# Kernel optimization log

Measured on AMD Instinct MI355X. Metric: run time of the kernel, lower is better.

The kernel has to match this reference:

```python
import jax, jax.numpy as jnp
import numpy as np

HIDDEN = 2048
HEADS = 16
HEAD_DIM = HIDDEN // HEADS
ROPE_BASE = 10000.0
BSZ, SEQ = 1, 2048
F32_MIN = jnp.finfo(jnp.float32).min


def setup_inputs() -> dict:
    key = jax.random.key(0)
    ks = jax.random.split(key, 5)
    hidden_states = jax.random.normal(ks[0], (BSZ, SEQ, HIDDEN), dtype=jnp.float32)
    # causal additive mask: 0 on/below diagonal, large negative above
    causal = jnp.tril(jnp.ones((SEQ, SEQ), dtype=bool))
    attention_mask = jnp.where(causal, 0.0, F32_MIN)[None, None, :, :].astype(jnp.float32)
    position_ids = jnp.broadcast_to(jnp.arange(SEQ, dtype=jnp.int32)[None, :], (BSZ, SEQ))
    scale = 1.0 / np.sqrt(HIDDEN)
    Wq = jax.random.normal(ks[1], (HIDDEN, HIDDEN), dtype=jnp.float32) * scale
    Wk = jax.random.normal(ks[2], (HIDDEN, HIDDEN), dtype=jnp.float32) * scale
    Wv = jax.random.normal(ks[3], (HIDDEN, HIDDEN), dtype=jnp.float32) * scale
    Wo = jax.random.normal(ks[4], (HIDDEN, HIDDEN), dtype=jnp.float32) * scale
    return {"hidden_states": hidden_states, "attention_mask": attention_mask,
            "position_ids": position_ids, "Wq": Wq, "Wk": Wk, "Wv": Wv, "Wo": Wo}


def _rotate_half(x):
    x1, x2 = jnp.split(x, 2, axis=-1)
    return jnp.concatenate([-x2, x1], axis=-1)


def _rope_cos_sin(position_ids, dtype):
    # [b, s] int -> cos/sin [b, 1, s, head_dim]
    inv_freq = 1.0 / (ROPE_BASE ** (jnp.arange(0, HEAD_DIM, 2, dtype=jnp.float32) / HEAD_DIM))
    freqs = position_ids.astype(jnp.float32)[..., None] * inv_freq  # [b, s, d/2]
    emb = jnp.concatenate([freqs, freqs], axis=-1)  # [b, s, d]
    return jnp.cos(emb)[:, None].astype(dtype), jnp.sin(emb)[:, None].astype(dtype)


def reference(hidden_states, attention_mask, position_ids, Wq, Wk, Wv, Wo):
    b, s, _ = hidden_states.shape

    def proj(W):  # [b, s, hidden] -> [b, h, s, d]
        return jnp.einsum('bsm,mn->bsn', hidden_states, W).reshape(b, s, HEADS, HEAD_DIM).transpose(0, 2, 1, 3)

    q, k, v = proj(Wq), proj(Wk), proj(Wv)
    cos, sin = _rope_cos_sin(position_ids, q.dtype)
    q = q * cos + _rotate_half(q) * sin
    k = k * cos + _rotate_half(k) * sin

    scores = jnp.einsum('bhqd,bhkd->bhqk', q, k) / np.sqrt(HEAD_DIM)
    scores = jnp.maximum(scores + attention_mask, F32_MIN)
    attn = jax.nn.softmax(scores.astype(jnp.float32), axis=-1).astype(q.dtype)
    out = jnp.einsum('bhqk,bhkd->bhqd', attn, v)  # [b, h, s, d]
    out = out.transpose(0, 2, 1, 3).reshape(b, s, HIDDEN)
    return jnp.einsum('bsm,mn->bsn', out, Wo)
```

## Files before the change

### kernel.cpp

```cpp
#include <hip/hip_runtime.h>
#include <hip/hip_bf16.h>
#include <math.h>

#define SEQn 2048
#define HID  2048
#define NH   16
#define HD   128

typedef __attribute__((ext_vector_type(8))) __bf16 bf16x8;
typedef __attribute__((ext_vector_type(4))) float  f32x4;

#define MFMA16(a,b,c) __builtin_amdgcn_mfma_f32_16x16x32_bf16((a),(b),(c),0,0,0)

__device__ __forceinline__ ushort f2bf(float f) {
  union { float f; unsigned u; } v; v.f = f;
  unsigned r = v.u + 0x7fffu + ((v.u >> 16) & 1u);
  return (ushort)(r >> 16);
}
__device__ __forceinline__ float bf2f(ushort u) {
  union { unsigned u; float f; } v; v.u = ((unsigned)u) << 16; return v.f;
}
__device__ __forceinline__ void split2(float x, ushort& h, ushort& l) {
  h = f2bf(x);
  l = f2bf(x - bf2f(h));
}
__device__ __forceinline__ void gl_lds16(const ushort* g, ushort* l) {
  __builtin_amdgcn_global_load_lds((const __attribute__((address_space(1))) unsigned int*)g,
                                   (__attribute__((address_space(3))) unsigned int*)l, 16, 0, 0);
}

__global__ void k_rope_tables(const int* __restrict__ pos,
                              float* __restrict__ cosT, float* __restrict__ sinT) {
  int t = threadIdx.x;
  int s = blockIdx.x * 4 + (t >> 6), i = t & 63;
  float p = (float)pos[s];
  float ex = (float)(2 * i) / 128.0f;
  float invf = 1.0f / powf(10000.0f, ex);
  float f = p * invf;
  cosT[s * 64 + i] = cosf(f);
  sinT[s * 64 + i] = sinf(f);
}

__global__ void k_split(const float* __restrict__ x,
                        ushort* __restrict__ hi, ushort* __restrict__ lo, int n4) {
  int i = blockIdx.x * blockDim.x + threadIdx.x;
  if (i >= n4) return;
  const float4 v = ((const float4*)x)[i];
  ushort4 h, l;
  split2(v.x, h.x, l.x); split2(v.y, h.y, l.y);
  split2(v.z, h.z, l.z); split2(v.w, h.w, l.w);
  ((ushort4*)hi)[i] = h; ((ushort4*)lo)[i] = l;
}

__global__ void k_splitT3(const float* __restrict__ W0, const float* __restrict__ W1,
                          const float* __restrict__ W2,
                          ushort* __restrict__ Th, ushort* __restrict__ Tl) {
  __shared__ float tile[32][33];
  const float* W = (blockIdx.z == 0) ? W0 : (blockIdx.z == 1) ? W1 : W2;
  ushort* Thz = Th + (size_t)blockIdx.z * HID * HID;
  ushort* Tlz = Tl + (size_t)blockIdx.z * HID * HID;
  int kb = blockIdx.x * 32, nb = blockIdx.y * 32;
  int tx = threadIdx.x, ty = threadIdx.y;
#pragma unroll
  for (int r = 0; r < 4; r++)
    tile[ty + r * 8][tx] = W[(size_t)(kb + ty + r * 8) * HID + nb + tx];
  __syncthreads();
#pragma unroll
  for (int r = 0; r < 4; r++) {
    int n = nb + ty + r * 8, k = kb + tx;
    ushort h, l; split2(tile[tx][ty + r * 8], h, l);
    Thz[(size_t)n * HID + k] = h;
    Tlz[(size_t)n * HID + k] = l;
  }
}

__global__ __launch_bounds__(512) void k_gemm_x3(
    const ushort* __restrict__ Ah, const ushort* __restrict__ Al,
    const ushort* __restrict__ Bh, const ushort* __restrict__ Bl,
    float* __restrict__ C) {
  __shared__ alignas(16) ushort lds[4][128 * 32];
  const int t = threadIdx.x, lane = t & 63, w = t >> 6;
  const int bm = blockIdx.y * 128, bn = blockIdx.x * 128;
  const size_t zb = (size_t)blockIdx.z * HID * HID;
  const int lr = lane & 15, lg = lane >> 4;
  const int sr = t >> 2, sc = (t & 3) * 8;
  const ushort* ga  = Ah + (size_t)(bm + sr) * HID + sc;
  const ushort* gal = Al + (size_t)(bm + sr) * HID + sc;
  const ushort* gb  = Bh + zb + (size_t)(bn + sr) * HID + sc;
  const ushort* gbl = Bl + zb + (size_t)(bn + sr) * HID + sc;
  ushort* l0 = &lds[0][w * 512];
  ushort* l1 = &lds[1][w * 512];
  ushort* l2 = &lds[2][w * 512];
  ushort* l3 = &lds[3][w * 512];
  const int wr = (w & 3) * 32, wc = (w >> 2) * 64;
  f32x4 acc[2][4] = {};
  for (int k0 = 0; k0 < HID; k0 += 32) {
    __syncthreads();
    gl_lds16(ga  + k0, l0);
    gl_lds16(gal + k0, l1);
    gl_lds16(gb  + k0, l2);
    gl_lds16(gbl + k0, l3);
    __syncthreads();
    bf16x8 a_h[2], a_l[2], b_h[4], b_l[4];
#pragma unroll
    for (int mi = 0; mi < 2; mi++) {
      int ro = (wr + mi * 16 + lr) * 32 + lg * 8;
      a_h[mi] = *(const bf16x8*)&lds[0][ro];
      a_l[mi] = *(const bf16x8*)&lds[1][ro];
    }
#pragma unroll
    for (int ni = 0; ni < 4; ni++) {
      int ro = (wc + ni * 16 + lr) * 32 + lg * 8;
      b_h[ni] = *(const bf16x8*)&lds[2][ro];
      b_l[ni] = *(const bf16x8*)&lds[3][ro];
    }
#pragma unroll
    for (int mi = 0; mi < 2; mi++)
#pragma unroll
      for (int ni = 0; ni < 4; ni++) {
        acc[mi][ni] = MFMA16(a_h[mi], b_h[ni], acc[mi][ni]);
        acc[mi][ni] = MFMA16(a_h[mi], b_l[ni], acc[mi][ni]);
        acc[mi][ni] = MFMA16(a_l[mi], b_h[ni], acc[mi][ni]);
      }
  }
  float* Cz = C + (size_t)blockIdx.z * SEQn * HID;
#pragma unroll
  for (int mi = 0; mi < 2; mi++)
#pragma unroll
    for (int ni = 0; ni < 4; ni++)
#pragma unroll
      for (int j = 0; j < 4; j++) {
        int row = bm + wr + mi * 16 + lg * 4 + j;
        int col = bn + wc + ni * 16 + lr;
        Cz[(size_t)row * HID + col] = acc[mi][ni][j];
      }
}

__global__ void k_rope_qk(const float* __restrict__ Qf, const float* __restrict__ Kf,
                          const float* __restrict__ cosT, const float* __restrict__ sinT,
                          ushort* __restrict__ Qhh, ushort* __restrict__ Qll,
                          ushort* __restrict__ Khh, ushort* __restrict__ Kll) {
  int t = threadIdx.x;
  int s = blockIdx.x * 4 + (t >> 6), h = blockIdx.y, d = t & 63;
  const float scale = 0.08838834764831845f;
  float c = cosT[s * 64 + d], sn = sinT[s * 64 + d];
  size_t in0  = (size_t)s * HID + h * HD + d;
  size_t out0 = ((size_t)h * SEQn + s) * HD + d;
  ushort hh, ll;
  {
    float q1 = Qf[in0] * scale, q2 = Qf[in0 + 64] * scale;
    split2(q1 * c - q2 * sn, hh, ll); Qhh[out0] = hh;      Qll[out0] = ll;
    split2(q2 * c + q1 * sn, hh, ll); Qhh[out0 + 64] = hh; Qll[out0 + 64] = ll;
  }
  {
    float k1 = Kf[in0], k2 = Kf[in0 + 64];
    split2(k1 * c - k2 * sn, hh, ll); Khh[out0] = hh;      Kll[out0] = ll;
    split2(k2 * c + k1 * sn, hh, ll); Khh[out0 + 64] = hh; Kll[out0 + 64] = ll;
  }
}

__global__ void k_transpose_v(const float* __restrict__ Vf,
                              ushort* __restrict__ Vth, ushort* __restrict__ Vtl) {
  __shared__ float tile[32][33];
  int h = blockIdx.x, db = blockIdx.y * 32, sb = blockIdx.z * 32;
  int tx = threadIdx.x, ty = threadIdx.y;
#pragma unroll
  for (int r = 0; r < 4; r++)
    tile[ty + r * 8][tx] = Vf[(size_t)(sb + ty + r * 8) * HID + h * HD + db + tx];
  __syncthreads();
#pragma unroll
  for (int r = 0; r < 4; r++) {
    int d = db + ty + r * 8, s = sb + tx;
    ushort hh, ll; split2(tile[tx][ty + r * 8], hh, ll);
    size_t o = ((size_t)h * HD + d) * SEQn + s;
    Vth[o] = hh; Vtl[o] = ll;
  }
}

__global__ __launch_bounds__(256) void k_attn(
    const ushort* __restrict__ Qhh, const ushort* __restrict__ Qll,
    const ushort* __restrict__ Khh, const ushort* __restrict__ Kll,
    const ushort* __restrict__ Vth, const ushort* __restrict__ Vtl,
    ushort* __restrict__ Ohi, ushort* __restrict__ Olo) {
  __shared__ alignas(16) ushort sKh[64 * 128];
  __shared__ alignas(16) ushort sKl[64 * 128];
  __shared__ alignas(16) ushort sVh[128 * 64];
  __shared__ alignas(16) ushort sVl[128 * 64];
  __shared__ alignas(16) ushort sP[4][16 * 72];
  const int t = threadIdx.x, lane = t & 63, w = t >> 6;
  const int flat = blockIdx.y * 32 + blockIdx.x;
  const int s_ = flat & 255, halfsel = flat >> 8;
  const int qt_ = s_ & 31, h_ = s_ >> 5;
  const int qt = halfsel ? (31 - qt_) : qt_;
  const int h  = halfsel ? (8 + h_) : h_;
  const int qb = qt * 64;
  const int lr = lane & 15, lg = lane >> 4;
  const int q0 = qb + w * 16;
  const size_t qoff = ((size_t)h * SEQn + q0 + lr) * HD + lg * 8;
  bf16x8 qh[4], ql[4];
#pragma unroll
  for (int ks = 0; ks < 4; ks++) {
    qh[ks] = *(const bf16x8*)(Qhh + qoff + ks * 32);
    ql[ks] = *(const bf16x8*)(Qll + qoff + ks * 32);
  }
  const int cc = (w << 6) | lane;
  const int rK = cc >> 4;
  const int cbK = (((cc & 15) << 4) ^ ((rK & 7) << 4)) >> 1;
  const size_t srcKo = (size_t)(h * SEQn + rK) * HD + cbK;
  const int rV = cc >> 3;
  const int cbV = (((cc & 7) << 4) ^ ((rV & 7) << 4)) >> 1;
  const size_t srcVo = (size_t)(h * HD + rV) * SEQn + cbV;

  f32x4 o[8] = {};
  float mrow[4], lrow[4];
#pragma unroll
  for (int j = 0; j < 4; j++) { mrow[j] = -INFINITY; lrow[j] = 0.f; }
  ushort* myp = &sP[w][0];

  for (int kv0 = 0; kv0 <= qb; kv0 += 64) {
    __syncthreads();
    {
      const ushort* gKh = Khh + srcKo + (size_t)kv0 * HD;
      const ushort* gKl = Kll + srcKo + (size_t)kv0 * HD;
      const ushort* gVh = Vth + srcVo + kv0;
      const ushort* gVl = Vtl + srcVo + kv0;
#pragma unroll
      for (int i = 0; i < 4; i++) {
        gl_lds16(gKh + (size_t)i * 16 * HD,  &sKh[(w + i * 4) * 512]);
        gl_lds16(gKl + (size_t)i * 16 * HD,  &sKl[(w + i * 4) * 512]);
        gl_lds16(gVh + (size_t)i * 32 * SEQn, &sVh[(w + i * 4) * 512]);
        gl_lds16(gVl + (size_t)i * 32 * SEQn, &sVl[(w + i * 4) * 512]);
      }
    }
    __syncthreads();
    f32x4 s4[4] = {};
    __builtin_amdgcn_s_setprio(1);
#pragma unroll
    for (int ni = 0; ni < 4; ni++) {
      const int kr = ni * 16 + lr;
      const int kbase = kr * 128;
      const int ksw = (kr & 7) << 4;
#pragma unroll
      for (int ks = 0; ks < 4; ks++) {
        const int off = kbase + (((ks * 64 + lg * 16) ^ ksw) >> 1);
        bf16x8 kh = *(const bf16x8*)&sKh[off];
        bf16x8 kl = *(const bf16x8*)&sKl[off];
        s4[ni] = MFMA16(qh[ks], kh, s4[ni]);
        s4[ni] = MFMA16(qh[ks], kl, s4[ni]);
        s4[ni] = MFMA16(ql[ks], kh, s4[ni]);
      }
    }
    __builtin_amdgcn_s_setprio(0);
    float sf[4];
    ushort pl[4][4];
#pragma unroll
    for (int j = 0; j < 4; j++) {
      const int row = q0 + lg * 4 + j;
      float sc[4];
#pragma unroll
      for (int ni = 0; ni < 4; ni++) {
        int col = kv0 + ni * 16 + lr;
        sc[ni] = (col <= row) ? s4[ni][j] : -INFINITY;
      }
      float rm = fmaxf(fmaxf(sc[0], sc[1]), fmaxf(sc[2], sc[3]));
#pragma unroll
      for (int off = 1; off < 16; off <<= 1) rm = fmaxf(rm, __shfl_xor(rm, off));
      float mn = fmaxf(mrow[j], rm);
      sf[j] = __expf(mrow[j] - mn);
      float rs = 0.f;
#pragma unroll
      for (int ni = 0; ni < 4; ni++) {
        float pv = __expf(sc[ni] - mn);
        rs += pv;
        ushort hh, ll; split2(pv, hh, ll);
        myp[(lg * 4 + j) * 72 + ni * 16 + lr] = hh;
        pl[j][ni] = ll;
      }
#pragma unroll
      for (int off = 1; off < 16; off <<= 1) rs += __shfl_xor(rs, off);
      lrow[j] = lrow[j] * sf[j] + rs;
      mrow[j] = mn;
    }
#pragma unroll
    for (int nn = 0; nn < 8; nn++) {
      o[nn][0] *= sf[0]; o[nn][1] *= sf[1]; o[nn][2] *= sf[2]; o[nn][3] *= sf[3];
    }
    bf16x8 p0h = *(const bf16x8*)&myp[lr * 72 + lg * 8];
    bf16x8 p1h = *(const bf16x8*)&myp[lr * 72 + lg * 8 + 32];
#pragma unroll
    for (int j = 0; j < 4; j++)
#pragma unroll
      for (int ni = 0; ni < 4; ni++)
        myp[(lg * 4 + j) * 72 + ni * 16 + lr] = pl[j][ni];
    bf16x8 p0l = *(const bf16x8*)&myp[lr * 72 + lg * 8];
    bf16x8 p1l = *(const bf16x8*)&myp[lr * 72 + lg * 8 + 32];
    __builtin_amdgcn_s_setprio(1);
#pragma unroll
    for (int nn = 0; nn < 8; nn++) {
      const int d = nn * 16 + lr;
      const int vbase = d * 64;
      const int vsw = (d & 7) << 4;
      const int o0 = vbase + (((lg * 16) ^ vsw) >> 1);
      const int o1 = vbase + (((lg * 16 + 64) ^ vsw) >> 1);
      bf16x8 vh0 = *(const bf16x8*)&sVh[o0];
      bf16x8 vl0 = *(const bf16x8*)&sVl[o0];
      bf16x8 vh1 = *(const bf16x8*)&sVh[o1];
      bf16x8 vl1 = *(const bf16x8*)&sVl[o1];
      o[nn] = MFMA16(p0h, vh0, o[nn]);
      o[nn] = MFMA16(p0h, vl0, o[nn]);
      o[nn] = MFMA16(p0l, vh0, o[nn]);
      o[nn] = MFMA16(p1h, vh1, o[nn]);
      o[nn] = MFMA16(p1h, vl1, o[nn]);
      o[nn] = MFMA16(p1l, vh1, o[nn]);
    }
    __builtin_amdgcn_s_setprio(0);
  }
#pragma unroll
  for (int nn = 0; nn < 8; nn++)
#pragma unroll
    for (int j = 0; j < 4; j++) {
      int row = q0 + lg * 4 + j;
      int col = h * HD + nn * 16 + lr;
      ushort hh, ll; split2(o[nn][j] / lrow[j], hh, ll);
      Ohi[(size_t)row * HID + col] = hh;
      Olo[(size_t)row * HID + col] = ll;
    }
}

extern "C" void kernel_launch(void* const* d_in, const int* in_sizes, int n_in,
                              void* d_out, int out_size, void* d_ws, size_t ws_size,
                              hipStream_t stream) {
  const float* Hf  = (const float*)d_in[0];
  const int*   pos = (const int*)d_in[2];
  const float* Wq  = (const float*)d_in[3];
  const float* Wk  = (const float*)d_in[4];
  const float* Wv  = (const float*)d_in[5];
  const float* Wo  = (const float*)d_in[6];

  char* ws = (char*)d_ws;
  const size_t SZ_TBL = (size_t)SEQn * 64 * 4;
  const size_t SZ_BF  = (size_t)SEQn * HID * 2;
  const size_t SZ_F   = (size_t)SEQn * HID * 4;
  const size_t PLANE  = (size_t)HID * HID;
  size_t off = 0;
  float*  cosT = (float*)(ws + off);  off += SZ_TBL;
  float*  sinT = (float*)(ws + off);  off += SZ_TBL;
  ushort* Hhi  = (ushort*)(ws + off); off += SZ_BF;
  ushort* Hlo  = (ushort*)(ws + off); off += SZ_BF;
  ushort* W3h  = (ushort*)(ws + off); off += 3 * SZ_BF;
  ushort* W3l  = (ushort*)(ws + off); off += 3 * SZ_BF;
  float*  QKVf = (float*)(ws + off);  off += 3 * SZ_F;
  float*  Qf = QKVf;
  float*  Kf = QKVf + (size_t)SEQn * HID;
  float*  Vf = QKVf + 2 * (size_t)SEQn * HID;
  ushort* Qhh = W3h;
  ushort* Qll = W3h + PLANE;
  ushort* Khh = W3h + 2 * PLANE;
  ushort* Kll = W3l;
  ushort* Vth = W3l + PLANE;
  ushort* Vtl = W3l + 2 * PLANE;
  ushort* Ohi = (ushort*)Kf;
  ushort* Olo = (ushort*)((char*)Kf + SZ_BF);

  const int n4 = SEQn * HID / 4;

  k_rope_tables<<<dim3(SEQn / 4), dim3(256), 0, stream>>>(pos, cosT, sinT);
  k_split<<<dim3(n4 / 256), dim3(256), 0, stream>>>(Hf, Hhi, Hlo, n4);

  k_splitT3<<<dim3(64, 64, 3), dim3(32, 8), 0, stream>>>(Wq, Wk, Wv, W3h, W3l);

  k_gemm_x3<<<dim3(16, 16, 3), dim3(512), 0, stream>>>(Hhi, Hlo, W3h, W3l, QKVf);

  k_rope_qk<<<dim3(SEQn / 4, NH), dim3(256), 0, stream>>>(Qf, Kf, cosT, sinT, Qhh, Qll, Khh, Kll);
  k_transpose_v<<<dim3(NH, 4, 64), dim3(32, 8), 0, stream>>>(Vf, Vth, Vtl);

  k_attn<<<dim3(SEQn / 64, NH), dim3(256), 0, stream>>>(Qhh, Qll, Khh, Kll, Vth, Vtl, Ohi, Olo);

  k_splitT3<<<dim3(64, 64, 1), dim3(32, 8), 0, stream>>>(Wo, Wo, Wo, W3h, W3l);
  k_gemm_x3<<<dim3(16, 16, 1), dim3(512), 0, stream>>>(Ohi, Olo, W3h, W3l, (float*)d_out);
}
```

Baseline: 518.1 us.

## Double-buffer LDS tiles in attention and output-projection GEMM to overlap loads

Adds ping-pong LDS buffers to the attention kernel for K and V tiles, and to a templated GEMM variant used only for the output projection. Each iteration now prefetches the next tile while computing on the current one, leaving a single barrier per iteration instead of two. The aim is to hide global-to-LDS load latency behind MFMA work. The attention kernel's LDS roughly doubles, to about 137KB per block, which may cut resident blocks per CU and reduce latency hiding from occupancy. The QKV GEMM keeps the original single-buffer path.

```diff
diff --git a/kernel.cpp b/kernel.cpp
--- a/kernel.cpp
+++ b/kernel.cpp
@@ -74,11 +74,12 @@
   }
 }
 
+template<int DB>
 __global__ __launch_bounds__(512) void k_gemm_x3(
     const ushort* __restrict__ Ah, const ushort* __restrict__ Al,
     const ushort* __restrict__ Bh, const ushort* __restrict__ Bl,
     float* __restrict__ C) {
-  __shared__ alignas(16) ushort lds[4][128 * 32];
+  __shared__ alignas(16) ushort lds[DB][4][4096];
   const int t = threadIdx.x, lane = t & 63, w = t >> 6;
   const int bm = blockIdx.y * 128, bn = blockIdx.x * 128;
   const size_t zb = (size_t)blockIdx.z * HID * HID;
@@ -88,31 +89,43 @@
   const ushort* gal = Al + (size_t)(bm + sr) * HID + sc;
   const ushort* gb  = Bh + zb + (size_t)(bn + sr) * HID + sc;
   const ushort* gbl = Bl + zb + (size_t)(bn + sr) * HID + sc;
-  ushort* l0 = &lds[0][w * 512];
-  ushort* l1 = &lds[1][w * 512];
-  ushort* l2 = &lds[2][w * 512];
-  ushort* l3 = &lds[3][w * 512];
   const int wr = (w & 3) * 32, wc = (w >> 2) * 64;
   f32x4 acc[2][4] = {};
+  int cur = 0;
+  if constexpr (DB == 2) {
+    gl_lds16(ga,  &lds[0][0][w * 512]);
+    gl_lds16(gal, &lds[0][1][w * 512]);
+    gl_lds16(gb,  &lds[0][2][w * 512]);
+    gl_lds16(gbl, &lds[0][3][w * 512]);
+  }
   for (int k0 = 0; k0 < HID; k0 += 32) {
     __syncthreads();
-    gl_lds16(ga  + k0, l0);
-    gl_lds16(gal + k0, l1);
-    gl_lds16(gb  + k0, l2);
-    gl_lds16(gbl + k0, l3);
-    __syncthreads();
+    if constexpr (DB == 2) {
+      if (k0 + 32 < HID) {
+        gl_lds16(ga  + k0 + 32, &lds[cur ^ 1][0][w * 512]);
+        gl_lds16(gal + k0 + 32, &lds[cur ^ 1][1][w * 512]);
+        gl_lds16(gb  + k0 + 32, &lds[cur ^ 1][2][w * 512]);
+        gl_lds16(gbl + k0 + 32, &lds[cur ^ 1][3][w * 512]);
+      }
+    } else {
+      gl_lds16(ga  + k0, &lds[0][0][w * 512]);
+      gl_lds16(gal + k0, &lds[0][1][w * 512]);
+      gl_lds16(gb  + k0, &lds[0][2][w * 512]);
+      gl_lds16(gbl + k0, &lds[0][3][w * 512]);
+      __syncthreads();
+    }
     bf16x8 a_h[2], a_l[2], b_h[4], b_l[4];
 #pragma unroll
     for (int mi = 0; mi < 2; mi++) {
       int ro = (wr + mi * 16 + lr) * 32 + lg * 8;
-      a_h[mi] = *(const bf16x8*)&lds[0][ro];
-      a_l[mi] = *(const bf16x8*)&lds[1][ro];
+      a_h[mi] = *(const bf16x8*)&lds[cur][0][ro];
+      a_l[mi] = *(const bf16x8*)&lds[cur][1][ro];
     }
 #pragma unroll
     for (int ni = 0; ni < 4; ni++) {
       int ro = (wc + ni * 16 + lr) * 32 + lg * 8;
-      b_h[ni] = *(const bf16x8*)&lds[2][ro];
-      b_l[ni] = *(const bf16x8*)&lds[3][ro];
+      b_h[ni] = *(const bf16x8*)&lds[cur][2][ro];
+      b_l[ni] = *(const bf16x8*)&lds[cur][3][ro];
     }
 #pragma unroll
     for (int mi = 0; mi < 2; mi++)
@@ -122,6 +135,7 @@
         acc[mi][ni] = MFMA16(a_h[mi], b_l[ni], acc[mi][ni]);
         acc[mi][ni] = MFMA16(a_l[mi], b_h[ni], acc[mi][ni]);
       }
+    if constexpr (DB == 2) cur ^= 1;
   }
   float* Cz = C + (size_t)blockIdx.z * SEQn * HID;
 #pragma unroll
@@ -182,11 +196,11 @@
     const ushort* __restrict__ Khh, const ushort* __restrict__ Kll,
     const ushort* __restrict__ Vth, const ushort* __restrict__ Vtl,
     ushort* __restrict__ Ohi, ushort* __restrict__ Olo) {
-  __shared__ alignas(16) ushort sKh[64 * 128];
-  __shared__ alignas(16) ushort sKl[64 * 128];
-  __shared__ alignas(16) ushort sVh[128 * 64];
-  __shared__ alignas(16) ushort sVl[128 * 64];
-  __shared__ alignas(16) ushort sP[4][16 * 72];
+  __shared__ alignas(16) ushort sKh[2][8192];
+  __shared__ alignas(16) ushort sKl[2][8192];
+  __shared__ alignas(16) ushort sVh[2][8192];
+  __shared__ alignas(16) ushort sVl[2][8192];
+  __shared__ alignas(16) ushort sP[4][1152];
   const int t = threadIdx.x, lane = t & 63, w = t >> 6;
   const int flat = blockIdx.y * 32 + blockIdx.x;
   const int s_ = flat & 255, halfsel = flat >> 8;
@@ -217,22 +231,36 @@
   for (int j = 0; j < 4; j++) { mrow[j] = -INFINITY; lrow[j] = 0.f; }
   ushort* myp = &sP[w][0];
 
+  {
+    const ushort* gKh = Khh + srcKo;
+    const ushort* gKl = Kll + srcKo;
+    const ushort* gVh = Vth + srcVo;
+    const ushort* gVl = Vtl + srcVo;
+#pragma unroll
+    for (int i = 0; i < 4; i++) {
+      gl_lds16(gKh + (size_t)i * 16 * HD,   &sKh[0][(w + i * 4) * 512]);
+      gl_lds16(gKl + (size_t)i * 16 * HD,   &sKl[0][(w + i * 4) * 512]);
+      gl_lds16(gVh + (size_t)i * 32 * SEQn, &sVh[0][(w + i * 4) * 512]);
+      gl_lds16(gVl + (size_t)i * 32 * SEQn, &sVl[0][(w + i * 4) * 512]);
+    }
+  }
+
   for (int kv0 = 0; kv0 <= qb; kv0 += 64) {
+    const int cur = (kv0 >> 6) & 1;
     __syncthreads();
-    {
-      const ushort* gKh = Khh + srcKo + (size_t)kv0 * HD;
-      const ushort* gKl = Kll + srcKo + (size_t)kv0 * HD;
-      const ushort* gVh = Vth + srcVo + kv0;
-      const ushort* gVl = Vtl + srcVo + kv0;
+    if (kv0 + 64 <= qb) {
+      const ushort* gKh = Khh + srcKo + (size_t)(kv0 + 64) * HD;
+      const ushort* gKl = Kll + srcKo + (size_t)(kv0 + 64) * HD;
+      const ushort* gVh = Vth + srcVo + kv0 + 64;
+      const ushort* gVl = Vtl + srcVo + kv0 + 64;
 #pragma unroll
       for (int i = 0; i < 4; i++) {
-        gl_lds16(gKh + (size_t)i * 16 * HD,  &sKh[(w + i * 4) * 512]);
-        gl_lds16(gKl + (size_t)i * 16 * HD,  &sKl[(w + i * 4) * 512]);
-        gl_lds16(gVh + (size_t)i * 32 * SEQn, &sVh[(w + i * 4) * 512]);
-        gl_lds16(gVl + (size_t)i * 32 * SEQn, &sVl[(w + i * 4) * 512]);
-      }
-    }
-    __syncthreads();
+        gl_lds16(gKh + (size_t)i * 16 * HD,   &sKh[cur ^ 1][(w + i * 4) * 512]);
+        gl_lds16(gKl + (size_t)i * 16 * HD,   &sKl[cur ^ 1][(w + i * 4) * 512]);
+        gl_lds16(gVh + (size_t)i * 32 * SEQn, &sVh[cur ^ 1][(w + i * 4) * 512]);
+        gl_lds16(gVl + (size_t)i * 32 * SEQn, &sVl[cur ^ 1][(w + i * 4) * 512]);
+      }
+    }
     f32x4 s4[4] = {};
     __builtin_amdgcn_s_setprio(1);
 #pragma unroll
@@ -243,8 +271,8 @@
 #pragma unroll
       for (int ks = 0; ks < 4; ks++) {
         const int off = kbase + (((ks * 64 + lg * 16) ^ ksw) >> 1);
-        bf16x8 kh = *(const bf16x8*)&sKh[off];
-        bf16x8 kl = *(const bf16x8*)&sKl[off];
+        bf16x8 kh = *(const bf16x8*)&sKh[cur][off];
+        bf16x8 kl = *(const bf16x8*)&sKl[cur][off];
         s4[ni] = MFMA16(qh[ks], kh, s4[ni]);
         s4[ni] = MFMA16(qh[ks], kl, s4[ni]);
         s4[ni] = MFMA16(ql[ks], kh, s4[ni]);
@@ -302,10 +330,10 @@
       const int vsw = (d & 7) << 4;
       const int o0 = vbase + (((lg * 16) ^ vsw) >> 1);
       const int o1 = vbase + (((lg * 16 + 64) ^ vsw) >> 1);
-      bf16x8 vh0 = *(const bf16x8*)&sVh[o0];
-      bf16x8 vl0 = *(const bf16x8*)&sVl[o0];
-      bf16x8 vh1 = *(const bf16x8*)&sVh[o1];
-      bf16x8 vl1 = *(const bf16x8*)&sVl[o1];
+      bf16x8 vh0 = *(const bf16x8*)&sVh[cur][o0];
+      bf16x8 vl0 = *(const bf16x8*)&sVl[cur][o0];
+      bf16x8 vh1 = *(const bf16x8*)&sVh[cur][o1];
+      bf16x8 vl1 = *(const bf16x8*)&sVl[cur][o1];
       o[nn] = MFMA16(p0h, vh0, o[nn]);
       o[nn] = MFMA16(p0h, vl0, o[nn]);
       o[nn] = MFMA16(p0l, vh0, o[nn]);
@@ -369,7 +397,7 @@
 
   k_splitT3<<<dim3(64, 64, 3), dim3(32, 8), 0, stream>>>(Wq, Wk, Wv, W3h, W3l);
 
-  k_gemm_x3<<<dim3(16, 16, 3), dim3(512), 0, stream>>>(Hhi, Hlo, W3h, W3l, QKVf);
+  k_gemm_x3<1><<<dim3(16, 16, 3), dim3(512), 0, stream>>>(Hhi, Hlo, W3h, W3l, QKVf);
 
   k_rope_qk<<<dim3(SEQn / 4, NH), dim3(256), 0, stream>>>(Qf, Kf, cosT, sinT, Qhh, Qll, Khh, Kll);
   k_transpose_v<<<dim3(NH, 4, 64), dim3(32, 8), 0, stream>>>(Vf, Vth, Vtl);
@@ -377,5 +405,5 @@
   k_attn<<<dim3(SEQn / 64, NH), dim3(256), 0, stream>>>(Qhh, Qll, Khh, Kll, Vth, Vtl, Ohi, Olo);
 
   k_splitT3<<<dim3(64, 64, 1), dim3(32, 8), 0, stream>>>(Wo, Wo, Wo, W3h, W3l);
-  k_gemm_x3<<<dim3(16, 16, 1), dim3(512), 0, stream>>>(Ohi, Olo, W3h, W3l, (float*)d_out);
-}
+  k_gemm_x3<2><<<dim3(16, 16, 1), dim3(512), 0, stream>>>(Ohi, Olo, W3h, W3l, (float*)d_out);
+}
```

Result: slower. 585.7 us (+13.1%).
